# Kernel tuning notes

Measured on AMD Instinct MI355X. Metric: run time of the kernel, lower is better.

## Reference

```python
import jax, jax.numpy as jnp
import numpy as np

B, S, M, E, H = 4, 2048, 1024, 8, 4096
CAP = 2 * (B * S) // E  # GShard top-2 capacity = 2*s/e = 2048


def setup_inputs() -> dict:
    key = jax.random.key(0)
    k = jax.random.split(key, 6)
    sc = 0.02
    return {
        "x": jax.random.normal(k[0], (B, S, M), jnp.float32),
        "wg": jax.random.normal(k[1], (M, E), jnp.float32) * sc,
        "w1": jax.random.normal(k[2], (E, M, H), jnp.float32) * sc,
        "b1": jnp.zeros((E, H), jnp.float32),
        "w2": jax.random.normal(k[3], (E, H, M), jnp.float32) * sc,
        "b2": jnp.zeros((E, M), jnp.float32),
    }


def top2gating(logits, capacity):
    # Faithful GShard/fairscale top2gating: logits [s, e]
    s, e = logits.shape
    gates = jax.nn.softmax(logits, axis=-1)
    idx1 = jnp.argmax(gates, axis=1)
    mask1 = jax.nn.one_hot(idx1, e, dtype=jnp.float32)
    logits2 = jnp.where(mask1 > 0, -jnp.inf, logits)
    idx2 = jnp.argmax(logits2, axis=1)
    mask2 = jax.nn.one_hot(idx2, e, dtype=jnp.float32)
    # positions within each expert's buffer
    loc1 = jnp.cumsum(mask1, axis=0) - 1.0
    loc2 = jnp.cumsum(mask2, axis=0) - 1.0 + jnp.sum(mask1, axis=0, keepdims=True)
    # load-balancing aux loss (computed before capacity drop, per fairscale)
    me = jnp.mean(gates, axis=0)
    ce = jnp.mean(mask1, axis=0)
    l_aux = jnp.mean(me * ce) * (e * e)
    # drop tokens over capacity
    mask1 = mask1 * (loc1 < capacity)
    mask2 = mask2 * (loc2 < capacity)
    loc1_s = jnp.sum(loc1 * mask1, axis=1).astype(jnp.int32)
    loc2_s = jnp.sum(loc2 * mask2, axis=1).astype(jnp.int32)
    gates1 = jnp.sum(gates * mask1, axis=1)
    gates2 = jnp.sum(gates * mask2, axis=1)
    denom = jnp.maximum(gates1 + gates2, 1e-9)
    gates1 = gates1 / denom
    gates2 = gates2 / denom
    # dense [s, e, c] combine weights (as in the original einsum formulation)
    oh1 = jax.nn.one_hot(loc1_s, capacity, dtype=jnp.float32)
    oh2 = jax.nn.one_hot(loc2_s, capacity, dtype=jnp.float32)
    combine = (gates1[:, None] * mask1)[:, :, None] * oh1[:, None, :] \
            + (gates2[:, None] * mask2)[:, :, None] * oh2[:, None, :]
    dispatch = combine > 0
    return l_aux, combine, dispatch


def reference(x, wg, w1, b1, w2, b2):
    d_model = x.shape[2]
    xf = x.reshape(-1, d_model)                      # [s, m]
    logits = xf @ wg                                 # [s, e]
    l_aux, combine, dispatch = top2gating(logits, CAP)
    # dispatch: dense one-hot scatter, as in torch.einsum('sec,sm->ecm')
    disp = jnp.einsum('sec,sm->ecm', dispatch.astype(xf.dtype), xf)
    # per-expert FFN (Linear -> ReLU -> Linear), vectorized over experts
    h = jax.nn.relu(jnp.einsum('ecm,emh->ech', disp, w1) + b1[:, None, :])
    eo = jnp.einsum('ech,ehm->ecm', h, w2) + b2[:, None, :]
    # combine: torch.einsum('sec,ecm->sm')
    out = jnp.einsum('sec,ecm->sm', combine, eo)
    return out.reshape(x.shape), l_aux
```

## Files before the change

kernel.cpp:

```cpp
#include <hip/hip_runtime.h>
#include <stdint.h>

typedef unsigned short u16;
typedef __attribute__((ext_vector_type(8))) short bf16x8;
typedef __attribute__((ext_vector_type(4))) float f32x4;

#define TOKENS 8192
#define DM 1024
#define NE 8
#define DH 4096
#define CAP 2048

__device__ __forceinline__ u16 f2bf(float f) {
  unsigned int u = __float_as_uint(f);
  u = u + 0x7FFFu + ((u >> 16) & 1u);
  return (u16)(u >> 16);
}

__device__ __forceinline__ void gll16(const void* g, void* l) {
  __builtin_amdgcn_global_load_lds(
      (const __attribute__((address_space(1))) unsigned int*)g,
      (__attribute__((address_space(3))) unsigned int*)l, 16, 0, 0);
}

__global__ __launch_bounds__(256) void gating_kernel(
    const float* __restrict__ x, const float* __restrict__ wg,
    int* __restrict__ idx1, int* __restrict__ idx2,
    float* __restrict__ g1r, float* __restrict__ g2r, float* __restrict__ me) {
  __shared__ float gsh[4][8];
  int lane = threadIdx.x & 63;
  int w = threadIdx.x >> 6;
  int t = blockIdx.x * 4 + w;
  const float* xr = x + (size_t)t * DM;
  double acc[8];
#pragma unroll
  for (int e = 0; e < 8; ++e) acc[e] = 0.0;
#pragma unroll
  for (int it = 0; it < 4; ++it) {
    float4 xv = ((const float4*)xr)[it * 64 + lane];
    int base = (it * 64 + lane) * 4;
    const float* wr = wg + (size_t)base * 8;
    float xs[4] = {xv.x, xv.y, xv.z, xv.w};
#pragma unroll
    for (int j = 0; j < 4; ++j)
#pragma unroll
      for (int e = 0; e < 8; ++e) acc[e] += (double)xs[j] * (double)wr[j * 8 + e];
  }
#pragma unroll
  for (int off = 32; off > 0; off >>= 1)
#pragma unroll
    for (int e = 0; e < 8; ++e) acc[e] += __shfl_down(acc[e], off);
  if (lane == 0) {
    float l[8];
#pragma unroll
    for (int e = 0; e < 8; ++e) l[e] = (float)acc[e];
    int i1 = 0;
    float v1 = l[0];
#pragma unroll
    for (int e = 1; e < 8; ++e)
      if (l[e] > v1) { v1 = l[e]; i1 = e; }
    int i2 = -1;
    float v2 = -3.4e38f;
#pragma unroll
    for (int e = 0; e < 8; ++e)
      if (e != i1 && l[e] > v2) { v2 = l[e]; i2 = e; }
    float s = 0.f;
    float p[8];
#pragma unroll
    for (int e = 0; e < 8; ++e) { p[e] = expf(l[e] - v1); s += p[e]; }
    float inv = 1.f / s;
    idx1[t] = i1;
    idx2[t] = i2;
    g1r[t] = inv;
    g2r[t] = expf(v2 - v1) * inv;
#pragma unroll
    for (int e = 0; e < 8; ++e) gsh[w][e] = p[e] * inv;
  }
  __syncthreads();
  if (threadIdx.x < 8) {
    int e = threadIdx.x;
    atomicAdd(&me[e], gsh[0][e] + gsh[1][e] + gsh[2][e] + gsh[3][e]);
  }
}

__global__ __launch_bounds__(1024) void scan_kernel(
    const int* __restrict__ idx1, const int* __restrict__ idx2,
    const float* __restrict__ g1r, const float* __restrict__ g2r,
    const float* __restrict__ me,
    int* __restrict__ slot1, int* __restrict__ slot2,
    float* __restrict__ g1n, float* __restrict__ g2n,
    int* __restrict__ slot2tok, float* __restrict__ laux) {
  __shared__ u16 c[16][1024];
  __shared__ u16 csum[16][32];
  __shared__ int tot[16];
  int tid = threadIdx.x;
  int i1[8], i2[8];
#pragma unroll
  for (int ctr = 0; ctr < 16; ++ctr) c[ctr][tid] = 0;
#pragma unroll
  for (int j = 0; j < 8; ++j) {
    int t = tid * 8 + j;
    i1[j] = idx1[t];
    i2[j] = idx2[t];
    c[i1[j]][tid]++;
    c[8 + i2[j]][tid]++;
  }
  __syncthreads();
  if (tid < 512) {
    int ctr = tid >> 5, ch = tid & 31;
    int s = 0;
#pragma unroll
    for (int i = 0; i < 32; ++i) s += c[ctr][ch * 32 + i];
    csum[ctr][ch] = (u16)s;
  }
  __syncthreads();
  if (tid < 16) {
    int run = 0;
#pragma unroll
    for (int ch = 0; ch < 32; ++ch) {
      int v = csum[tid][ch];
      csum[tid][ch] = (u16)run;
      run += v;
    }
    tot[tid] = run;
  }
  __syncthreads();
  if (tid < 512) {
    int ctr = tid >> 5, ch = tid & 31;
    int run = csum[ctr][ch];
#pragma unroll
    for (int i = 0; i < 32; ++i) {
      int v = c[ctr][ch * 32 + i];
      c[ctr][ch * 32 + i] = (u16)run;
      run += v;
    }
  }
  __syncthreads();
#pragma unroll
  for (int j = 0; j < 8; ++j) {
    int t = tid * 8 + j;
    int e1 = i1[j], e2 = i2[j];
    int L1 = c[e1][tid]++;
    int L2 = c[8 + e2][tid]++;
    L2 += tot[e2];
    bool kv1 = L1 < CAP, kv2 = L2 < CAP;
    float G1 = kv1 ? g1r[t] : 0.f;
    float G2 = kv2 ? g2r[t] : 0.f;
    float den = fmaxf(G1 + G2, 1e-9f);
    g1n[t] = G1 / den;
    g2n[t] = G2 / den;
    int s1 = kv1 ? (e1 * CAP + L1) : -1;
    int s2 = kv2 ? (e2 * CAP + L2) : -1;
    slot1[t] = s1;
    slot2[t] = s2;
    if (kv1) slot2tok[s1] = t;
    if (kv2) slot2tok[s2] = t;
  }
  if (tid == 0) {
    double a = 0.0;
    for (int e = 0; e < 8; ++e)
      a += ((double)me[e] / 8192.0) * ((double)tot[e] / 8192.0);
    laux[0] = (float)(a * 8.0);
  }
}

__global__ void transpose_kernel(const float* __restrict__ src, u16* __restrict__ dst,
                                 int R, int C) {
  __shared__ float tile[32][33];
  int tx = threadIdx.x, ty = threadIdx.y;
  int r0 = blockIdx.y * 32, c0 = blockIdx.x * 32;
  const float* s = src + (size_t)blockIdx.z * R * C;
  u16* d = dst + (size_t)blockIdx.z * R * C;
#pragma unroll
  for (int i = 0; i < 32; i += 8) tile[ty + i][tx] = s[(size_t)(r0 + ty + i) * C + c0 + tx];
  __syncthreads();
#pragma unroll
  for (int i = 0; i < 32; i += 8)
    d[(size_t)(c0 + ty + i) * R + r0 + tx] = f2bf(tile[tx][ty + i]);
}

__global__ void gather_kernel(const float* __restrict__ x, const int* __restrict__ slot2tok,
                              u16* __restrict__ xe) {
  int slot = blockIdx.y * CAP + blockIdx.x;
  int tok = slot2tok[slot];
  int tid = threadIdx.x;
  u16 o[8];
  if (tok >= 0) {
    const float4* xr = (const float4*)(x + (size_t)tok * DM);
    float4 a = xr[tid * 2], b = xr[tid * 2 + 1];
    o[0] = f2bf(a.x); o[1] = f2bf(a.y); o[2] = f2bf(a.z); o[3] = f2bf(a.w);
    o[4] = f2bf(b.x); o[5] = f2bf(b.y); o[6] = f2bf(b.z); o[7] = f2bf(b.w);
  } else {
#pragma unroll
    for (int j = 0; j < 8; ++j) o[j] = 0;
  }
  *(uint4*)(xe + (size_t)slot * DM + tid * 8) = *(const uint4*)o;
}

#define BAR()                              \
  {                                        \
    asm volatile("" ::: "memory");         \
    __builtin_amdgcn_s_barrier();          \
    asm volatile("" ::: "memory");         \
  }
#define VMCNT(n) asm volatile("s_waitcnt vmcnt(" #n ")" ::: "memory")

template <int RELU, int OUTBF16>
__global__ __launch_bounds__(512, 2) void gemm_kernel(
    const u16* __restrict__ A, const u16* __restrict__ Bt,
    const float* __restrict__ bias, void* __restrict__ Cv,
    int MO, int NO, int K) {
  __shared__ __align__(16) u16 As[2][256 * 64];
  __shared__ __align__(16) u16 Bs[2][256 * 64];
  const int tid = threadIdx.x;
  const int lane = tid & 63, wid = tid >> 6;
  const int wm = wid >> 2, wn = wid & 3;
  const int eb = blockIdx.z;
  const size_t Ks2 = (size_t)K * 2;
  const char* Ag = (const char*)(A + (size_t)eb * MO * K + (size_t)blockIdx.y * 256 * K);
  const char* Bg = (const char*)(Bt + (size_t)eb * NO * K + (size_t)blockIdx.x * 256 * K);
  const int rl = tid >> 3;
  const int sb = ((tid & 7) * 16) ^ ((rl & 7) << 4);
  Ag += (size_t)rl * Ks2 + sb;
  Bg += (size_t)rl * Ks2 + sb;
  char* AsB = ((char*)As) + tid * 16;
  char* BsB = ((char*)Bs) + tid * 16;
  const u16* AsE = &As[0][0];
  const u16* BsE = &Bs[0][0];
  const int fr = lane & 15, kg8 = (lane >> 4) * 8;
  const int swz = (fr & 7) << 3;

#define STAGE_A(BUF_, REG_, KT_) \
  gll16(Ag + (size_t)((REG_)*64) * Ks2 + (size_t)(KT_)*128, AsB + (BUF_)*32768 + (REG_)*8192)
#define STAGE_B(BUF_, REG_, KT_) \
  gll16(Bg + (size_t)((REG_)*64) * Ks2 + (size_t)(KT_)*128, BsB + (BUF_)*32768 + (REG_)*8192)
#define LDA(BUF_, M_, K_) \
  (*(const bf16x8*)&AsE[(BUF_)*16384 + (wm * 128 + (M_)*16 + fr) * 64 + (((K_)*32 + kg8) ^ swz)])
#define LDB(BUF_, N_, K_) \
  (*(const bf16x8*)&BsE[(BUF_)*16384 + (wn * 64 + (N_)*16 + fr) * 64 + (((K_)*32 + kg8) ^ swz)])
#define MFMA_Q(MB_, NB_)                                                            \
  _Pragma("unroll") for (int m = 0; m < 4; ++m)                                     \
  _Pragma("unroll") for (int n = 0; n < 2; ++n)                                     \
  _Pragma("unroll") for (int k = 0; k < 2; ++k)                                     \
      acc[(MB_) + m][(NB_) + n] = __builtin_amdgcn_mfma_f32_16x16x32_bf16(          \
          areg[m][k], breg[(NB_) + n][k], acc[(MB_) + m][(NB_) + n], 0, 0, 0)

  f32x4 acc[8][4];
#pragma unroll
  for (int i = 0; i < 8; ++i)
#pragma unroll
    for (int j = 0; j < 4; ++j) acc[i][j] = {0.f, 0.f, 0.f, 0.f};
  bf16x8 areg[4][2], breg[4][2];

  STAGE_B(0, 0, 0); STAGE_B(0, 1, 0); STAGE_B(0, 2, 0); STAGE_B(0, 3, 0);
  STAGE_A(0, 0, 0); STAGE_A(0, 2, 0); STAGE_A(0, 1, 0); STAGE_A(0, 3, 0);
  VMCNT(2);
  BAR();

#define PHASE_SET(CUR_, NXT_, ST_)                                                  \
  {                                                                                 \
                              \
    _Pragma("unroll") for (int m = 0; m < 4; ++m) {                                 \
      areg[m][0] = LDA(CUR_, m, 0); areg[m][1] = LDA(CUR_, m, 1);                   \
    }                                                                               \
    _Pragma("unroll") for (int n = 0; n < 2; ++n) {                                 \
      breg[n][0] = LDB(CUR_, n, 0); breg[n][1] = LDB(CUR_, n, 1);                   \
    }                                                                               \
    STAGE_B(NXT_, 0, ST_); STAGE_B(NXT_, 1, ST_);                                   \
    BAR();                                                                          \
    __builtin_amdgcn_s_setprio(1); MFMA_Q(0, 0); __builtin_amdgcn_s_setprio(0);     \
    BAR();                                                                          \
            \
    _Pragma("unroll") for (int n = 2; n < 4; ++n) {                                 \
      breg[n][0] = LDB(CUR_, n, 0); breg[n][1] = LDB(CUR_, n, 1);                   \
    }                                                                               \
    STAGE_B(NXT_, 2, ST_); STAGE_B(NXT_, 3, ST_);                                   \
    VMCNT(4);                                                                       \
    BAR();                                                                          \
    __builtin_amdgcn_s_setprio(1); MFMA_Q(0, 2); __builtin_amdgcn_s_setprio(0);     \
    BAR();                                                                          \
                        \
    _Pragma("unroll") for (int m = 0; m < 4; ++m) {                                 \
      areg[m][0] = LDA(CUR_, 4 + m, 0); areg[m][1] = LDA(CUR_, 4 + m, 1);           \
    }                                                                               \
    STAGE_A(NXT_, 0, ST_); STAGE_A(NXT_, 2, ST_);                                   \
    BAR();                                                                          \
    __builtin_amdgcn_s_setprio(1); MFMA_Q(4, 0); __builtin_amdgcn_s_setprio(0);     \
    BAR();                                                                          \
                         \
    STAGE_A(NXT_, 1, ST_); STAGE_A(NXT_, 3, ST_);                                   \
    VMCNT(2);                                                                       \
    BAR();                                                                          \
    __builtin_amdgcn_s_setprio(1); MFMA_Q(4, 2); __builtin_amdgcn_s_setprio(0);     \
    BAR();                                                                          \
  }

  const int NT = K >> 6;
  for (int t = 0; t < NT; t += 2) {
    const int st1 = t + 1;
    const int st2 = (t + 2 < NT) ? (t + 2) : (NT - 1);
    PHASE_SET(0, 1, st1);
    PHASE_SET(1, 0, st2);
  }

  const int row0 = blockIdx.y * 256 + wm * 128 + (kg8 >> 3) * 4;
  const int col0 = blockIdx.x * 256 + wn * 64 + fr;
  const float* be = bias + (size_t)eb * NO;
  size_t cbase = (size_t)eb * MO * NO;
#pragma unroll
  for (int m = 0; m < 8; ++m) {
#pragma unroll
    for (int n = 0; n < 4; ++n) {
      int col = col0 + n * 16;
      float bv = be[col];
#pragma unroll
      for (int r = 0; r < 4; ++r) {
        int row = row0 + m * 16 + r;
        float v = acc[m][n][r] + bv;
        if (RELU) v = fmaxf(v, 0.f);
        if (OUTBF16)
          ((u16*)Cv)[cbase + (size_t)row * NO + col] = f2bf(v);
        else
          ((float*)Cv)[cbase + (size_t)row * NO + col] = v;
      }
    }
  }
#undef PHASE_SET
#undef STAGE_A
#undef STAGE_B
#undef LDA
#undef LDB
#undef MFMA_Q
}

__global__ void combine_kernel(const float* __restrict__ eo,
                               const float* __restrict__ g1n, const float* __restrict__ g2n,
                               const int* __restrict__ slot1, const int* __restrict__ slot2,
                               float* __restrict__ out) {
  int t = blockIdx.x, tid = threadIdx.x;
  float g1 = g1n[t], g2 = g2n[t];
  int s1 = slot1[t], s2 = slot2[t];
  float4 o = make_float4(0.f, 0.f, 0.f, 0.f);
  if (s1 >= 0) {
    float4 a = ((const float4*)(eo + (size_t)s1 * DM))[tid];
    o.x = g1 * a.x; o.y = g1 * a.y; o.z = g1 * a.z; o.w = g1 * a.w;
  }
  if (s2 >= 0) {
    float4 b = ((const float4*)(eo + (size_t)s2 * DM))[tid];
    o.x += g2 * b.x; o.y += g2 * b.y; o.z += g2 * b.z; o.w += g2 * b.w;
  }
  ((float4*)(out + (size_t)t * DM))[tid] = o;
}

extern "C" void kernel_launch(void* const* d_in, const int* in_sizes, int n_in,
                              void* d_out, int out_size, void* d_ws, size_t ws_size,
                              hipStream_t stream) {
  const float* x = (const float*)d_in[0];
  const float* wg = (const float*)d_in[1];
  const float* w1 = (const float*)d_in[2];
  const float* b1 = (const float*)d_in[3];
  const float* w2 = (const float*)d_in[4];
  const float* b2 = (const float*)d_in[5];
  float* out = (float*)d_out;

  const size_t SZ_WT1 = (size_t)NE * DH * DM * 2;
  const size_t SZ_WT2 = (size_t)NE * DM * DH * 2;
  const size_t SZ_XE = (size_t)NE * CAP * DM * 2;
  const size_t SZ_H = (size_t)NE * CAP * DH * 2;
  const size_t SZ_TOK = (size_t)TOKENS * 4;

  char* p = (char*)d_ws;
  u16* wt1 = (u16*)p;
  float* eo = (float*)p;            p += SZ_WT1;
  u16* wt2 = (u16*)p;               p += SZ_WT2;
  u16* xe = (u16*)p;                p += SZ_XE;
  u16* h = (u16*)p;                 p += SZ_H;
  int* idx1 = (int*)p;              p += SZ_TOK;
  int* idx2 = (int*)p;              p += SZ_TOK;
  int* slot1 = (int*)p;             p += SZ_TOK;
  int* slot2 = (int*)p;             p += SZ_TOK;
  float* g1r = (float*)p;           p += SZ_TOK;
  float* g2r = (float*)p;           p += SZ_TOK;
  float* g1n = (float*)p;           p += SZ_TOK;
  float* g2n = (float*)p;           p += SZ_TOK;
  int* slot2tok = (int*)p;          p += (size_t)NE * CAP * 4;
  float* me = (float*)p;            p += 256;
  if ((size_t)(p - (char*)d_ws) > ws_size) return;

  hipMemsetAsync(me, 0, 32, stream);
  hipMemsetAsync(slot2tok, 0xFF, (size_t)NE * CAP * 4, stream);

  gating_kernel<<<TOKENS / 4, 256, 0, stream>>>(x, wg, idx1, idx2, g1r, g2r, me);
  scan_kernel<<<1, 1024, 0, stream>>>(idx1, idx2, g1r, g2r, me, slot1, slot2, g1n, g2n,
                                      slot2tok, out + (size_t)TOKENS * DM);
  transpose_kernel<<<dim3(DH / 32, DM / 32, NE), dim3(32, 8), 0, stream>>>(w1, wt1, DM, DH);
  transpose_kernel<<<dim3(DM / 32, DH / 32, NE), dim3(32, 8), 0, stream>>>(w2, wt2, DH, DM);
  gather_kernel<<<dim3(CAP, NE), 128, 0, stream>>>(x, slot2tok, xe);
  gemm_kernel<1, 1><<<dim3(DH / 256, CAP / 256, NE), 512, 0, stream>>>(xe, wt1, b1, (void*)h,
                                                                       CAP, DH, DM);
  gemm_kernel<0, 0><<<dim3(DM / 256, CAP / 256, NE), 512, 0, stream>>>(h, wt2, b2, (void*)eo,
                                                                       CAP, DM, DH);
  combine_kernel<<<TOKENS, 256, 0, stream>>>(eo, g1n, g2n, slot1, slot2, out);
}
```

Before: 523.7 us.

## Remap workgroups across XCDs and deepen B-tile prefetch pipeline in expert GEMM

Remaps the linear workgroup ID so that consecutive tiles of the same expert and row block land on the same XCD, to improve L2 reuse of shared A/B panels. It also restructures the global-to-LDS pipeline: B is prefetched two K-steps ahead into the current buffer after its last read, while A is loaded one step ahead, so more loads are in flight. The MFMA loop order changes to k-outer. The remap assumes the workgroup count is divisible by 8, and the new buffer reuse relies on barrier ordering being correct.

```diff
diff --git a/kernel.cpp b/kernel.cpp
--- a/kernel.cpp
+++ b/kernel.cpp
@@ -215,10 +215,20 @@
   const int tid = threadIdx.x;
   const int lane = tid & 63, wid = tid >> 6;
   const int wm = wid >> 2, wn = wid & 3;
-  const int eb = blockIdx.z;
+
+  const int gx = gridDim.x, gy = gridDim.y;
+  const int nwg = gx * gy * gridDim.z;
+  const int L = (blockIdx.z * gy + blockIdx.y) * gx + blockIdx.x;
+  const int cpx = nwg >> 3;
+  const int Ls = (L & 7) * cpx + (L >> 3);
+  const int bx = Ls % gx;
+  const int tq = Ls / gx;
+  const int by = tq % gy;
+  const int eb = tq / gy;
+
   const size_t Ks2 = (size_t)K * 2;
-  const char* Ag = (const char*)(A + (size_t)eb * MO * K + (size_t)blockIdx.y * 256 * K);
-  const char* Bg = (const char*)(Bt + (size_t)eb * NO * K + (size_t)blockIdx.x * 256 * K);
+  const char* Ag = (const char*)(A + (size_t)eb * MO * K + (size_t)by * 256 * K);
+  const char* Bg = (const char*)(Bt + (size_t)eb * NO * K + (size_t)bx * 256 * K);
   const int rl = tid >> 3;
   const int sb = ((tid & 7) * 16) ^ ((rl & 7) << 4);
   Ag += (size_t)rl * Ks2 + sb;
@@ -239,9 +249,9 @@
 #define LDB(BUF_, N_, K_) \
   (*(const bf16x8*)&BsE[(BUF_)*16384 + (wn * 64 + (N_)*16 + fr) * 64 + (((K_)*32 + kg8) ^ swz)])
 #define MFMA_Q(MB_, NB_)                                                            \
+  _Pragma("unroll") for (int k = 0; k < 2; ++k)                                     \
   _Pragma("unroll") for (int m = 0; m < 4; ++m)                                     \
   _Pragma("unroll") for (int n = 0; n < 2; ++n)                                     \
-  _Pragma("unroll") for (int k = 0; k < 2; ++k)                                     \
       acc[(MB_) + m][(NB_) + n] = __builtin_amdgcn_mfma_f32_16x16x32_bf16(          \
           areg[m][k], breg[(NB_) + n][k], acc[(MB_) + m][(NB_) + n], 0, 0, 0)
 
@@ -252,59 +262,64 @@
     for (int j = 0; j < 4; ++j) acc[i][j] = {0.f, 0.f, 0.f, 0.f};
   bf16x8 areg[4][2], breg[4][2];
 
+  const int NT = K >> 6;
   STAGE_B(0, 0, 0); STAGE_B(0, 1, 0); STAGE_B(0, 2, 0); STAGE_B(0, 3, 0);
-  STAGE_A(0, 0, 0); STAGE_A(0, 2, 0); STAGE_A(0, 1, 0); STAGE_A(0, 3, 0);
-  VMCNT(2);
+  STAGE_A(0, 0, 0); STAGE_A(0, 1, 0); STAGE_A(0, 2, 0); STAGE_A(0, 3, 0);
+  {
+    const int s1 = (1 < NT) ? 1 : 0;
+    STAGE_B(1, 0, s1); STAGE_B(1, 1, s1); STAGE_B(1, 2, s1); STAGE_B(1, 3, s1);
+  }
+  VMCNT(4);
   BAR();
 
-#define PHASE_SET(CUR_, NXT_, ST_)                                                  \
+#define PHASE_SET(CUR_, NXT_, STA_, STB_)                                           \
   {                                                                                 \
-                              \
+                        \
     _Pragma("unroll") for (int m = 0; m < 4; ++m) {                                 \
       areg[m][0] = LDA(CUR_, m, 0); areg[m][1] = LDA(CUR_, m, 1);                   \
     }                                                                               \
     _Pragma("unroll") for (int n = 0; n < 2; ++n) {                                 \
       breg[n][0] = LDB(CUR_, n, 0); breg[n][1] = LDB(CUR_, n, 1);                   \
     }                                                                               \
-    STAGE_B(NXT_, 0, ST_); STAGE_B(NXT_, 1, ST_);                                   \
+    STAGE_A(NXT_, 0, STA_); STAGE_A(NXT_, 1, STA_);                                 \
+    STAGE_A(NXT_, 2, STA_); STAGE_A(NXT_, 3, STA_);                                 \
     BAR();                                                                          \
     __builtin_amdgcn_s_setprio(1); MFMA_Q(0, 0); __builtin_amdgcn_s_setprio(0);     \
     BAR();                                                                          \
-            \
+                                                            \
     _Pragma("unroll") for (int n = 2; n < 4; ++n) {                                 \
       breg[n][0] = LDB(CUR_, n, 0); breg[n][1] = LDB(CUR_, n, 1);                   \
     }                                                                               \
-    STAGE_B(NXT_, 2, ST_); STAGE_B(NXT_, 3, ST_);                                   \
-    VMCNT(4);                                                                       \
     BAR();                                                                          \
     __builtin_amdgcn_s_setprio(1); MFMA_Q(0, 2); __builtin_amdgcn_s_setprio(0);     \
     BAR();                                                                          \
-                        \
+       \
     _Pragma("unroll") for (int m = 0; m < 4; ++m) {                                 \
       areg[m][0] = LDA(CUR_, 4 + m, 0); areg[m][1] = LDA(CUR_, 4 + m, 1);           \
     }                                                                               \
-    STAGE_A(NXT_, 0, ST_); STAGE_A(NXT_, 2, ST_);                                   \
+    STAGE_B(CUR_, 0, STB_); STAGE_B(CUR_, 1, STB_);                                 \
     BAR();                                                                          \
     __builtin_amdgcn_s_setprio(1); MFMA_Q(4, 0); __builtin_amdgcn_s_setprio(0);     \
     BAR();                                                                          \
-                         \
-    STAGE_A(NXT_, 1, ST_); STAGE_A(NXT_, 3, ST_);                                   \
-    VMCNT(2);                                                                       \
+      \
+    STAGE_B(CUR_, 2, STB_); STAGE_B(CUR_, 3, STB_);                                 \
+    VMCNT(4);                                                                       \
     BAR();                                                                          \
     __builtin_amdgcn_s_setprio(1); MFMA_Q(4, 2); __builtin_amdgcn_s_setprio(0);     \
     BAR();                                                                          \
   }
 
-  const int NT = K >> 6;
   for (int t = 0; t < NT; t += 2) {
-    const int st1 = t + 1;
-    const int st2 = (t + 2 < NT) ? (t + 2) : (NT - 1);
-    PHASE_SET(0, 1, st1);
-    PHASE_SET(1, 0, st2);
-  }
-
-  const int row0 = blockIdx.y * 256 + wm * 128 + (kg8 >> 3) * 4;
-  const int col0 = blockIdx.x * 256 + wn * 64 + fr;
+    const int sa1 = (t + 1 < NT) ? t + 1 : NT - 1;
+    const int sb1 = (t + 2 < NT) ? t + 2 : NT - 1;
+    const int sa2 = (t + 2 < NT) ? t + 2 : NT - 1;
+    const int sb2 = (t + 3 < NT) ? t + 3 : NT - 1;
+    PHASE_SET(0, 1, sa1, sb1);
+    PHASE_SET(1, 0, sa2, sb2);
+  }
+
+  const int row0 = by * 256 + wm * 128 + (kg8 >> 3) * 4;
+  const int col0 = bx * 256 + wn * 64 + fr;
   const float* be = bias + (size_t)eb * NO;
   size_t cbase = (size_t)eb * MO * NO;
 #pragma unroll
```

Result: faster. 470.9 us (-10.1%).
